# Kernel tuning notes

Measured on AMD Instinct MI355X. Metric: run time of the kernel, lower is better.

Reference implementation:

```python
import jax, jax.numpy as jnp
from jax import lax
import numpy as np

EPS_LN = 1e-5
EPS_BN = 1e-5
NEG_SLOPE = 0.01  # MONAI UnetResBlock leaky relu slope


def conv3d(x, w, b=None, padding=0, dilation=1, groups=1):
    # x: [B,C,D1,D2,D3], w: [O, I/groups, k,k,k]
    pads = [(padding, padding)] * 3
    y = lax.conv_general_dilated(x, w, (1, 1, 1), pads,
                                 rhs_dilation=(dilation,) * 3,
                                 dimension_numbers=('NCDHW', 'OIDHW', 'NCDHW'),
                                 feature_group_count=groups)
    if b is not None:
        y = y + b[None, :, None, None, None]
    return y


def _trilinear(x_flat, z, y, xw, D, H, W):
    # x_flat: [B,C,S]; z,y,xw: [B,S] float sample coords. Zero padding outside.
    z0 = jnp.floor(z); y0 = jnp.floor(y); x0 = jnp.floor(xw)
    tz = z - z0; ty = y - y0; tx = xw - x0
    iz0 = z0.astype(jnp.int32); iy0 = y0.astype(jnp.int32); ix0 = x0.astype(jnp.int32)
    gather = jax.vmap(lambda xf, i: jnp.take(xf, i, axis=1))  # over batch
    out = jnp.zeros_like(x_flat)
    for dz in (0, 1):
        for dy in (0, 1):
            for dx in (0, 1):
                zi = iz0 + dz; yi = iy0 + dy; xi = ix0 + dx
                wgt = ((tz if dz else 1.0 - tz) * (ty if dy else 1.0 - ty)
                       * (tx if dx else 1.0 - tx))
                valid = ((zi >= 0) & (zi < D) & (yi >= 0) & (yi < H)
                         & (xi >= 0) & (xi < W))
                idx = (jnp.clip(zi, 0, D - 1) * H + jnp.clip(yi, 0, H - 1)) * W \
                      + jnp.clip(xi, 0, W - 1)
                g = gather(x_flat, idx)  # [B,C,S]
                out = out + g * (wgt * valid)[:, None, :]
    return out


def deform_conv3d(x, off_w, off_b, w, b):
    # DCNv1-style 3D deformable conv, kernel 3x3x3, stride 1, pad 1.
    B, C, D, H, W = x.shape
    S = D * H * W
    off = conv3d(x, off_w, off_b, padding=1)          # [B, 3*27, D,H,W]
    off = off.reshape(B, 27, 3, S)                    # per-tap (dz,dy,dx)
    gz, gy, gx = jnp.meshgrid(jnp.arange(D), jnp.arange(H), jnp.arange(W), indexing='ij')
    gz = gz.reshape(-1).astype(x.dtype)
    gy = gy.reshape(-1).astype(x.dtype)
    gx = gx.reshape(-1).astype(x.dtype)
    x_flat = x.reshape(B, C, S)
    out = jnp.zeros((B, w.shape[0], S), x.dtype)
    k = 0
    for kd in (-1, 0, 1):
        for kh in (-1, 0, 1):
            for kw in (-1, 0, 1):
                z = gz[None, :] + kd + off[:, k, 0]
                y = gy[None, :] + kh + off[:, k, 1]
                xc = gx[None, :] + kw + off[:, k, 2]
                val = _trilinear(x_flat, z, y, xc, D, H, W)  # [B,C,S]
                out = out + jnp.einsum('oc,bcs->bos', w[:, :, kd + 1, kh + 1, kw + 1], val)
                k += 1
    out = out + b[None, :, None]
    return out.reshape(B, w.shape[0], D, H, W)


def _leaky(v):
    return jnp.where(v >= 0, v, NEG_SLOPE * v)


def _bn(v, s, b_, m, var):
    inv = lax.rsqrt(var + EPS_BN)
    return (v - m[None, :, None, None, None]) * (s * inv)[None, :, None, None, None] \
        + b_[None, :, None, None, None]


def reference(x, ln_s, ln_b, gamma,
              p1_w, p1_b, p2_w, p2_b,
              c0_w, c0_b, cs_w, cs_b,
              off_w, off_b, dc_w, dc_b,
              c1_w, c1_b,
              u1_w, bn1_s, bn1_b, bn1_m, bn1_v,
              u2_w, bn2_s, bn2_b, bn2_m, bn2_v,
              pr_w, pr_b):
    B, C, H, W, D = x.shape
    tok = x.reshape(B, C, -1).transpose(0, 2, 1)  # [B, N, C]
    # LayerNorm over C
    mu = jnp.mean(tok, axis=-1, keepdims=True)
    var = jnp.mean((tok - mu) ** 2, axis=-1, keepdims=True)
    xn = (tok - mu) * lax.rsqrt(var + EPS_LN) * ln_s + ln_b
    # _Attention3d_deform
    v = xn.transpose(0, 2, 1).reshape(B, C, H, W, D)
    shortcut = v
    v = conv3d(v, p1_w, p1_b)                 # proj_1 (1x1x1)
    v = jax.nn.gelu(v, approximate=False)
    # _3d_deform spatial gating unit
    u = v
    a = conv3d(v, c0_w, c0_b, padding=2, groups=C)              # 5x5x5 depthwise
    a = conv3d(a, cs_w, cs_b, padding=9, dilation=3, groups=C)  # 7x7x7 dil=3 depthwise
    a = deform_conv3d(a, off_w, off_b, dc_w, dc_b)
    a = conv3d(a, c1_w, c1_b)                 # 1x1x1
    v = u * a
    v = conv3d(v, p2_w, p2_b) + shortcut      # proj_2 + residual
    epa = v.reshape(B, C, -1).transpose(0, 2, 1)
    feat = tok + gamma * epa                  # [B, N, C]
    skip = feat.reshape(B, H, W, D, C).transpose(0, 4, 1, 2, 3)  # [B,C,H,W,D]
    # UnetResBlock (conv-bn-lrelu-conv-bn + residual, lrelu), eval-mode BN
    h = conv3d(skip, u1_w, padding=1)
    h = _leaky(_bn(h, bn1_s, bn1_b, bn1_m, bn1_v))
    h = conv3d(h, u2_w, padding=1)
    h = _bn(h, bn2_s, bn2_b, bn2_m, bn2_v)
    attn = _leaky(h + skip)
    # projconv: Dropout3d is identity in eval; 1x1x1 conv
    out = skip + conv3d(attn, pr_w, pr_b)
    return out


def setup_inputs() -> dict:
    key = jax.random.key(0)
    ks = jax.random.split(key, 16)
    C, Bv, S = 48, 2, 32

    def w(k, shape, s=0.05):
        return jax.random.normal(k, shape, jnp.float32) * s

    return {
        'x': jax.random.normal(ks[0], (Bv, C, S, S, S), jnp.float32),
        'ln_s': jnp.ones((C,), jnp.float32), 'ln_b': jnp.zeros((C,), jnp.float32),
        'gamma': jnp.full((C,), 0.1, jnp.float32),
        'p1_w': w(ks[1], (C, C, 1, 1, 1)), 'p1_b': jnp.zeros((C,), jnp.float32),
        'p2_w': w(ks[2], (C, C, 1, 1, 1)), 'p2_b': jnp.zeros((C,), jnp.float32),
        'c0_w': w(ks[3], (C, 1, 5, 5, 5)), 'c0_b': jnp.zeros((C,), jnp.float32),
        'cs_w': w(ks[4], (C, 1, 7, 7, 7)), 'cs_b': jnp.zeros((C,), jnp.float32),
        'off_w': w(ks[5], (81, C, 3, 3, 3), 0.01), 'off_b': jnp.zeros((81,), jnp.float32),
        'dc_w': w(ks[6], (C, C, 3, 3, 3)), 'dc_b': jnp.zeros((C,), jnp.float32),
        'c1_w': w(ks[7], (C, C, 1, 1, 1)), 'c1_b': jnp.zeros((C,), jnp.float32),
        'u1_w': w(ks[8], (C, C, 3, 3, 3)),
        'bn1_s': jnp.ones((C,), jnp.float32), 'bn1_b': jnp.zeros((C,), jnp.float32),
        'bn1_m': jnp.zeros((C,), jnp.float32), 'bn1_v': jnp.ones((C,), jnp.float32),
        'u2_w': w(ks[9], (C, C, 3, 3, 3)),
        'bn2_s': jnp.ones((C,), jnp.float32), 'bn2_b': jnp.zeros((C,), jnp.float32),
        'bn2_m': jnp.zeros((C,), jnp.float32), 'bn2_v': jnp.ones((C,), jnp.float32),
        'pr_w': w(ks[10], (C, C, 1, 1, 1)), 'pr_b': jnp.zeros((C,), jnp.float32),
    }
```

## Files before the change

kernel.cpp:

```cpp
#include <hip/hip_runtime.h>
#include <hip/hip_fp16.h>
#include <math.h>

#define CCH 48
#define SDIM 32
#define SVOL (SDIM*SDIM*SDIM)
#define NB 2

typedef _Float16 half2_t __attribute__((ext_vector_type(2)));
typedef _Float16 half4_t __attribute__((ext_vector_type(4)));
typedef float float4_t __attribute__((ext_vector_type(4)));

static __device__ __forceinline__ float dot2f(half2_t a, half2_t b, float c) {
#if __has_builtin(__builtin_amdgcn_fdot2)
    return __builtin_amdgcn_fdot2(a, b, c, false);
#else
    return c + (float)a[0] * (float)b[0] + (float)a[1] * (float)b[1];
#endif
}


__global__ __launch_bounds__(256)
void reshape_mfma_off_kernel(const float* __restrict__ w, half4_t* __restrict__ wA) {
    int e = blockIdx.x * 256 + threadIdx.x;
    if (e < 31104) {
        int row = e & 15;
        int kq = (e >> 4) & 3;
        int ks = (e / 64) % 3;
        int mt = (e / 192) % 6;
        int tap = e / 1152;
        int o = mt * 16 + row;
        half4_t v;
        #pragma unroll
        for (int h = 0; h < 4; h++) {
            int ci = ks * 16 + kq * 4 + h;
            float val = (o < 81) ? w[((size_t)o * CCH + ci) * 27 + tap] : 0.f;
            v[h] = (_Float16)val;
        }
        wA[e] = v;
    }
}

__global__ __launch_bounds__(256)
void reshape_mfma48_kernel(const float* __restrict__ w, half4_t* __restrict__ wA) {
    int e = blockIdx.x * 256 + threadIdx.x;
    if (e < 15552) {
        int row = e & 15;
        int kq = (e >> 4) & 3;
        int ks = (e / 64) % 3;
        int mt = (e / 192) % 3;
        int tap = e / 576;
        int o = mt * 16 + row;
        half4_t v;
        #pragma unroll
        for (int h = 0; h < 4; h++) {
            int ci = ks * 16 + kq * 4 + h;
            v[h] = (_Float16)w[((size_t)o * CCH + ci) * 27 + tap];
        }
        wA[e] = v;
    }
}

__global__ __launch_bounds__(256)
void reshape_mfma_dc_kernel(const float* __restrict__ w, half4_t* __restrict__ wA) {
    int e = blockIdx.x * 256 + threadIdx.x;
    if (e < 15552) {
        int row = e & 15;
        int kq = (e >> 4) & 3;
        int mt = (e / 64) % 3;
        int tap = (e / 192) % 27;
        int gc = e / 5184;
        int o = mt * 16 + row;
        half4_t v;
        #pragma unroll
        for (int h = 0; h < 4; h++) {
            int ci = gc * 16 + kq * 4 + h;
            v[h] = (_Float16)w[((size_t)o * CCH + ci) * 27 + tap];
        }
        wA[e] = v;
    }
}

__global__ __launch_bounds__(256)
void t1x1_pair_kernel(const float* __restrict__ w, half2_t* __restrict__ wt) {
    int i = blockIdx.x * 256 + threadIdx.x;
    if (i < 24 * CCH) {
        int o = i % CCH, cp = i / CCH;
        wt[i] = half2_t{ (_Float16)w[o * CCH + 2 * cp], (_Float16)w[o * CCH + 2 * cp + 1] };
    }
}

__global__ __launch_bounds__(256)
void t1x1_kernel(const float* __restrict__ w, float* __restrict__ wt) {
    int i = blockIdx.x * 256 + threadIdx.x;
    if (i < CCH * CCH) { int ci = i / CCH, o = i % CCH; wt[i] = w[o * CCH + ci]; }
}

__global__ __launch_bounds__(64)
void cb_kernel(const float* __restrict__ c1w, const float* __restrict__ c1b,
               const float* __restrict__ dcb, float* __restrict__ cb) {
    int o = threadIdx.x;
    if (o < CCH) {
        float v = c1b[o];
        for (int ci = 0; ci < CCH; ci++) v += c1w[o * CCH + ci] * dcb[ci];
        cb[o] = v;
    }
}

__global__ __launch_bounds__(256)
void ln_kernel(const float* __restrict__ x, const float* __restrict__ ln_s,
               const float* __restrict__ ln_b, float* __restrict__ xn,
               half2_t* __restrict__ xnp) {
    int s = blockIdx.x * 256 + threadIdx.x;
    int b = blockIdx.y;
    const float* xb = x + (size_t)b * CCH * SVOL + s;
    float v[CCH];
    float mu = 0.f;
    #pragma unroll
    for (int c = 0; c < CCH; c++) { v[c] = xb[c * SVOL]; mu += v[c]; }
    mu *= (1.0f / CCH);
    float var = 0.f;
    #pragma unroll
    for (int c = 0; c < CCH; c++) { float d = v[c] - mu; var += d * d; }
    var *= (1.0f / CCH);
    float inv = rsqrtf(var + 1e-5f);
    float* o = xn + (size_t)b * CCH * SVOL + s;
    float nv[CCH];
    #pragma unroll
    for (int c = 0; c < CCH; c++) { nv[c] = (v[c] - mu) * inv * ln_s[c] + ln_b[c]; o[c * SVOL] = nv[c]; }
    half2_t* xp = xnp + (size_t)b * 24 * SVOL + s;
    #pragma unroll
    for (int cp = 0; cp < 24; cp++)
        xp[(size_t)cp * SVOL] = half2_t{ (_Float16)nv[2 * cp], (_Float16)nv[2 * cp + 1] };
}

__global__ __launch_bounds__(256, 4)
void p1_gelu_kernel(const half2_t* __restrict__ xnp, const half2_t* __restrict__ wt,
                    const float* __restrict__ bias, float* __restrict__ u) {
    int tid = threadIdx.x;
    int g = blockIdx.y, b = blockIdx.z;
    int s = blockIdx.x * 256 + tid;
    const half2_t* xb = xnp + (size_t)b * 24 * SVOL + s;
    float acc[12];
    #pragma unroll
    for (int o = 0; o < 12; o++) acc[o] = bias[g * 12 + o];
    for (int cp = 0; cp < 24; cp++) {
        half2_t v2 = xb[(size_t)cp * SVOL];
        const half2_t* wr = wt + cp * CCH + g * 12;
        #pragma unroll
        for (int o = 0; o < 12; o++) acc[o] = dot2f(v2, wr[o], acc[o]);
    }
    float* ub = u + (size_t)b * CCH * SVOL + s + (size_t)(g * 12) * SVOL;
    #pragma unroll
    for (int o = 0; o < 12; o++) {
        float a = acc[o];
        ub[o * SVOL] = 0.5f * a * (1.0f + erff(a * 0.70710678118654752f));
    }
}

__global__ __launch_bounds__(256, 4)
void dw5_kernel(const float* __restrict__ in, const float* __restrict__ w,
                const float* __restrict__ bias, float* __restrict__ out) {
    int tid = threadIdx.x;
    int c = blockIdx.y, b = blockIdx.z;
    const float* wc = w + c * 125;
    int bx = blockIdx.x;
    int yx = (bx >> 1) * 256 + tid;
    int z0 = (bx & 1) * 16;
    int y = yx >> 5, xx = yx & 31;
    const float* ib = in + ((size_t)b * CCH + c) * SVOL;
    float acc[16];
    float bv = bias[c];
    #pragma unroll
    for (int z = 0; z < 16; z++) acc[z] = bv;
    for (int ty = 0; ty < 5; ty++) {
        int yy = y + ty - 2; if (yy < 0 || yy >= 32) continue;
        for (int tx = 0; tx < 5; tx++) {
            int xv = xx + tx - 2; if (xv < 0 || xv >= 32) continue;
            const float* col = ib + yy * 32 + xv;
            float cv[20];
            #pragma unroll
            for (int j = 0; j < 20; j++) {
                int zz = z0 - 2 + j;
                cv[j] = (zz >= 0 && zz < 32) ? col[(size_t)zz * 1024] : 0.f;
            }
            #pragma unroll
            for (int tz = 0; tz < 5; tz++) {
                float wv = wc[(tz * 5 + ty) * 5 + tx];
                #pragma unroll
                for (int z = 0; z < 16; z++) acc[z] += wv * cv[z + tz];
            }
        }
    }
    float* ob = out + ((size_t)b * CCH + c) * SVOL + y * 32 + xx;
    #pragma unroll
    for (int z = 0; z < 16; z++) ob[(size_t)(z0 + z) * 1024] = acc[z];
}

__global__ __launch_bounds__(256, 4)
void dw7_kernel(const float* __restrict__ in, const float* __restrict__ w,
                const float* __restrict__ bias, float* __restrict__ out) {
    int tid = threadIdx.x;
    int c = blockIdx.y, b = blockIdx.z;
    const float* wc = w + c * 343;
    int bx = blockIdx.x;
    int yx = (bx >> 1) * 256 + tid;
    int z0 = (bx & 1) * 16;
    int y = yx >> 5, xx = yx & 31;
    const float* ib = in + ((size_t)b * CCH + c) * SVOL;
    float acc[16];
    float bv = bias[c];
    #pragma unroll
    for (int z = 0; z < 16; z++) acc[z] = bv;
    for (int ty = 0; ty < 7; ty++) {
        int yy = y + 3 * (ty - 3); if (yy < 0 || yy >= 32) continue;
        for (int tx = 0; tx < 7; tx++) {
            int xv = xx + 3 * (tx - 3); if (xv < 0 || xv >= 32) continue;
            const float* col = ib + yy * 32 + xv;
            float cv[34];
            #pragma unroll
            for (int j = 0; j < 34; j++) {
                int zz = z0 - 9 + j;
                cv[j] = (zz >= 0 && zz < 32) ? col[(size_t)zz * 1024] : 0.f;
            }
            #pragma unroll
            for (int tz = 0; tz < 7; tz++) {
                float wv = wc[(tz * 7 + ty) * 7 + tx];
                #pragma unroll
                for (int z = 0; z < 16; z++) acc[z] += wv * cv[z + 3 * tz];
            }
        }
    }
    float* ob = out + ((size_t)b * CCH + c) * SVOL + y * 32 + xx;
    #pragma unroll
    for (int z = 0; z < 16; z++) ob[(size_t)(z0 + z) * 1024] = acc[z];
}

__global__ __launch_bounds__(256)
void transpose_pack_kernel(const float* __restrict__ a1, __half* __restrict__ a1h) {
    __shared__ float tile[CCH * 65];
    int tid = threadIdx.x;
    int b = blockIdx.y;
    int s0 = blockIdx.x * 64;
    const float* ib = a1 + (size_t)b * CCH * SVOL + s0;
    for (int i = tid; i < CCH * 64; i += 256) {
        int c = i >> 6, p = i & 63;
        tile[c * 65 + p] = ib[(size_t)c * SVOL + p];
    }
    __syncthreads();
    __half* ob = a1h + ((size_t)b * SVOL + s0) * CCH;
    for (int i = tid; i < 64 * CCH; i += 256) {
        int p = i / CCH, c = i % CCH;
        ob[i] = __float2half(tile[c * 65 + p]);
    }
}

__global__ __launch_bounds__(256, 4)
void offconv_mfma_kernel(const __half* __restrict__ a1h, const half4_t* __restrict__ wA,
                         float* __restrict__ off) {
    __shared__ __half halo[216 * 52];
    int tid = threadIdx.x;
    int t = blockIdx.x;
    int b = blockIdx.y;
    int tz0 = (t >> 6) * 4, ty0 = ((t >> 3) & 7) * 4, tx0 = (t & 7) * 4;
    const __half* ab = a1h + (size_t)b * SVOL * CCH;
    for (int idx = tid; idx < 216 * 24; idx += 256) {
        int hpos = idx / 24, kp = idx % 24;
        int hz = hpos / 36, hy = (hpos / 6) % 6, hx = hpos % 6;
        int gz = tz0 + hz - 1, gy = ty0 + hy - 1, gx = tx0 + hx - 1;
        unsigned int v = 0u;
        if (gz >= 0 && gz < 32 && gy >= 0 && gy < 32 && gx >= 0 && gx < 32) {
            int s = (gz * 32 + gy) * 32 + gx;
            v = *reinterpret_cast<const unsigned int*>(ab + (size_t)s * CCH + kp * 2);
        }
        *reinterpret_cast<unsigned int*>(&halo[hpos * 52 + kp * 2]) = v;
    }
    __syncthreads();
    int wave = tid >> 6, lane = tid & 63;
    int col = lane & 15;
    int kq = lane >> 4;
    int py = col >> 2, px = col & 3;
    int pz = wave;
    float4_t acc[6];
    #pragma unroll
    for (int m = 0; m < 6; m++) acc[m] = (float4_t)0.f;
    for (int tap = 0; tap < 27; tap++) {
        int dz = tap / 9, dy = (tap / 3) % 3, dx = tap % 3;
        int hbase = ((pz + dz) * 36 + (py + dy) * 6 + (px + dx)) * 52 + kq * 4;
        half4_t bf0 = *reinterpret_cast<const half4_t*>(&halo[hbase]);
        half4_t bf1 = *reinterpret_cast<const half4_t*>(&halo[hbase + 16]);
        half4_t bf2 = *reinterpret_cast<const half4_t*>(&halo[hbase + 32]);
        #pragma unroll
        for (int mt = 0; mt < 6; mt++) {
            int fb = (tap * 6 + mt) * 12 + kq;
            half4_t a0 = wA[(size_t)fb * 16 + col];
            half4_t a1 = wA[(size_t)(fb + 4) * 16 + col];
            half4_t a2 = wA[(size_t)(fb + 8) * 16 + col];
            acc[mt] = __builtin_amdgcn_mfma_f32_16x16x16f16(a0, bf0, acc[mt], 0, 0, 0);
            acc[mt] = __builtin_amdgcn_mfma_f32_16x16x16f16(a1, bf1, acc[mt], 0, 0, 0);
            acc[mt] = __builtin_amdgcn_mfma_f32_16x16x16f16(a2, bf2, acc[mt], 0, 0, 0);
        }
    }
    int sg = ((tz0 + pz) * 32 + ty0 + py) * 32 + tx0 + px;
    float* ob = off + (size_t)b * 81 * SVOL + sg;
    #pragma unroll
    for (int mt = 0; mt < 6; mt++) {
        #pragma unroll
        for (int r = 0; r < 4; r++) {
            int orow = mt * 16 + kq * 4 + r;
            if (orow < 81) ob[(size_t)orow * SVOL] = acc[mt][r];
        }
    }
}

__global__ __launch_bounds__(256, 4)
void u1_mfma_kernel(const __half* __restrict__ skh, const half4_t* __restrict__ wA,
                    const float* __restrict__ bs, const float* __restrict__ bb,
                    const float* __restrict__ bm, const float* __restrict__ bv,
                    __half* __restrict__ h1h) {
    __shared__ __half halo[216 * 52];
    int tid = threadIdx.x;
    int t = blockIdx.x;
    int b = blockIdx.y;
    int tz0 = (t >> 6) * 4, ty0 = ((t >> 3) & 7) * 4, tx0 = (t & 7) * 4;
    const __half* ab = skh + (size_t)b * SVOL * CCH;
    for (int idx = tid; idx < 216 * 24; idx += 256) {
        int hpos = idx / 24, kp = idx % 24;
        int hz = hpos / 36, hy = (hpos / 6) % 6, hx = hpos % 6;
        int gz = tz0 + hz - 1, gy = ty0 + hy - 1, gx = tx0 + hx - 1;
        unsigned int v = 0u;
        if (gz >= 0 && gz < 32 && gy >= 0 && gy < 32 && gx >= 0 && gx < 32) {
            int s = (gz * 32 + gy) * 32 + gx;
            v = *reinterpret_cast<const unsigned int*>(ab + (size_t)s * CCH + kp * 2);
        }
        *reinterpret_cast<unsigned int*>(&halo[hpos * 52 + kp * 2]) = v;
    }
    __syncthreads();
    int wave = tid >> 6, lane = tid & 63;
    int col = lane & 15;
    int kq = lane >> 4;
    int py = col >> 2, px = col & 3;
    int pz = wave;
    float4_t acc[3];
    #pragma unroll
    for (int m = 0; m < 3; m++) acc[m] = (float4_t)0.f;
    for (int tap = 0; tap < 27; tap++) {
        int dz = tap / 9, dy = (tap / 3) % 3, dx = tap % 3;
        int hbase = ((pz + dz) * 36 + (py + dy) * 6 + (px + dx)) * 52 + kq * 4;
        half4_t bf0 = *reinterpret_cast<const half4_t*>(&halo[hbase]);
        half4_t bf1 = *reinterpret_cast<const half4_t*>(&halo[hbase + 16]);
        half4_t bf2 = *reinterpret_cast<const half4_t*>(&halo[hbase + 32]);
        #pragma unroll
        for (int mt = 0; mt < 3; mt++) {
            int fb = (tap * 3 + mt) * 12 + kq;
            half4_t a0 = wA[(size_t)fb * 16 + col];
            half4_t a1 = wA[(size_t)(fb + 4) * 16 + col];
            half4_t a2 = wA[(size_t)(fb + 8) * 16 + col];
            acc[mt] = __builtin_amdgcn_mfma_f32_16x16x16f16(a0, bf0, acc[mt], 0, 0, 0);
            acc[mt] = __builtin_amdgcn_mfma_f32_16x16x16f16(a1, bf1, acc[mt], 0, 0, 0);
            acc[mt] = __builtin_amdgcn_mfma_f32_16x16x16f16(a2, bf2, acc[mt], 0, 0, 0);
        }
    }
    int sg = ((tz0 + pz) * 32 + ty0 + py) * 32 + tx0 + px;
    __half* ob = h1h + ((size_t)b * SVOL + sg) * CCH;
    #pragma unroll
    for (int mt = 0; mt < 3; mt++) {
        float hv[4];
        #pragma unroll
        for (int r = 0; r < 4; r++) {
            int orow = mt * 16 + kq * 4 + r;
            float inv = rsqrtf(bv[orow] + 1e-5f);
            float h = (acc[mt][r] - bm[orow]) * (bs[orow] * inv) + bb[orow];
            hv[r] = h >= 0.f ? h : 0.01f * h;
        }
        half2_t* po = reinterpret_cast<half2_t*>(ob + mt * 16 + kq * 4);
        po[0] = half2_t{ (_Float16)hv[0], (_Float16)hv[1] };
        po[1] = half2_t{ (_Float16)hv[2], (_Float16)hv[3] };
    }
}

__global__ __launch_bounds__(256, 4)
void u2_mfma_kernel(const __half* __restrict__ h1h, const float* __restrict__ skip,
                    const half4_t* __restrict__ wA,
                    const float* __restrict__ bs, const float* __restrict__ bb,
                    const float* __restrict__ bm, const float* __restrict__ bv,
                    __half* __restrict__ attnh) {
    __shared__ __half halo[216 * 52];
    int tid = threadIdx.x;
    int t = blockIdx.x;
    int b = blockIdx.y;
    int tz0 = (t >> 6) * 4, ty0 = ((t >> 3) & 7) * 4, tx0 = (t & 7) * 4;
    const __half* ab = h1h + (size_t)b * SVOL * CCH;
    for (int idx = tid; idx < 216 * 24; idx += 256) {
        int hpos = idx / 24, kp = idx % 24;
        int hz = hpos / 36, hy = (hpos / 6) % 6, hx = hpos % 6;
        int gz = tz0 + hz - 1, gy = ty0 + hy - 1, gx = tx0 + hx - 1;
        unsigned int v = 0u;
        if (gz >= 0 && gz < 32 && gy >= 0 && gy < 32 && gx >= 0 && gx < 32) {
            int s = (gz * 32 + gy) * 32 + gx;
            v = *reinterpret_cast<const unsigned int*>(ab + (size_t)s * CCH + kp * 2);
        }
        *reinterpret_cast<unsigned int*>(&halo[hpos * 52 + kp * 2]) = v;
    }
    __syncthreads();
    int wave = tid >> 6, lane = tid & 63;
    int col = lane & 15;
    int kq = lane >> 4;
    int py = col >> 2, px = col & 3;
    int pz = wave;
    float4_t acc[3];
    #pragma unroll
    for (int m = 0; m < 3; m++) acc[m] = (float4_t)0.f;
    for (int tap = 0; tap < 27; tap++) {
        int dz = tap / 9, dy = (tap / 3) % 3, dx = tap % 3;
        int hbase = ((pz + dz) * 36 + (py + dy) * 6 + (px + dx)) * 52 + kq * 4;
        half4_t bf0 = *reinterpret_cast<const half4_t*>(&halo[hbase]);
        half4_t bf1 = *reinterpret_cast<const half4_t*>(&halo[hbase + 16]);
        half4_t bf2 = *reinterpret_cast<const half4_t*>(&halo[hbase + 32]);
        #pragma unroll
        for (int mt = 0; mt < 3; mt++) {
            int fb = (tap * 3 + mt) * 12 + kq;
            half4_t a0 = wA[(size_t)fb * 16 + col];
            half4_t a1 = wA[(size_t)(fb + 4) * 16 + col];
            half4_t a2 = wA[(size_t)(fb + 8) * 16 + col];
            acc[mt] = __builtin_amdgcn_mfma_f32_16x16x16f16(a0, bf0, acc[mt], 0, 0, 0);
            acc[mt] = __builtin_amdgcn_mfma_f32_16x16x16f16(a1, bf1, acc[mt], 0, 0, 0);
            acc[mt] = __builtin_amdgcn_mfma_f32_16x16x16f16(a2, bf2, acc[mt], 0, 0, 0);
        }
    }
    int sg = ((tz0 + pz) * 32 + ty0 + py) * 32 + tx0 + px;
    const float* sk = skip + (size_t)b * CCH * SVOL + sg;
    __half* ob = attnh + ((size_t)b * SVOL + sg) * CCH;
    #pragma unroll
    for (int mt = 0; mt < 3; mt++) {
        float av[4];
        #pragma unroll
        for (int r = 0; r < 4; r++) {
            int orow = mt * 16 + kq * 4 + r;
            float inv = rsqrtf(bv[orow] + 1e-5f);
            float h = (acc[mt][r] - bm[orow]) * (bs[orow] * inv) + bb[orow];
            float a = h + sk[(size_t)orow * SVOL];
            av[r] = a >= 0.f ? a : 0.01f * a;
        }
        half2_t* po = reinterpret_cast<half2_t*>(ob + mt * 16 + kq * 4);
        po[0] = half2_t{ (_Float16)av[0], (_Float16)av[1] };
        po[1] = half2_t{ (_Float16)av[2], (_Float16)av[3] };
    }
}

struct h8v { half2_t a, b, c, d; };

__global__ __launch_bounds__(64)
void deform_mfma_kernel(const __half* __restrict__ a1h, const float* __restrict__ off,
                        const float* __restrict__ off_b,
                        const half4_t* __restrict__ wA, float* __restrict__ out) {
    __shared__ __half vbuf[2][64][20];
    int lane = threadIdx.x;
    int gc = blockIdx.y;
    int b = blockIdx.z;
    int col = lane & 15, kq = lane >> 4;
    int s = blockIdx.x * 64 + lane;
    int z = s >> 10, y = (s >> 5) & 31, xx = s & 31;
    const __half* abase = a1h + (size_t)b * SVOL * CCH + gc * 16;
    const float* ob = off + (size_t)b * 81 * SVOL + s;
    float4_t acc[3][4];
    #pragma unroll
    for (int m = 0; m < 3; m++)
        #pragma unroll
        for (int c = 0; c < 4; c++) acc[m][c] = (float4_t)0.f;
    for (int k = 0; k < 27; k++) {
        int kd = k / 9 - 1, kh = (k / 3) % 3 - 1, kw = k % 3 - 1;
        float zf = (float)(z + kd) + ob[(size_t)(k * 3 + 0) * SVOL] + off_b[k * 3 + 0];
        float yf = (float)(y + kh) + ob[(size_t)(k * 3 + 1) * SVOL] + off_b[k * 3 + 1];
        float xf = (float)(xx + kw) + ob[(size_t)(k * 3 + 2) * SVOL] + off_b[k * 3 + 2];
        float z0 = floorf(zf), y0 = floorf(yf), x0 = floorf(xf);
        float tz = zf - z0, ty = yf - y0, tx = xf - x0;
        int iz0 = (int)z0, iy0 = (int)y0, ix0 = (int)x0;
        half2_t val2[8];
        #pragma unroll
        for (int j = 0; j < 8; j++) val2[j] = (half2_t)(_Float16)0;
        #pragma unroll
        for (int corner = 0; corner < 8; corner++) {
            int dz = corner >> 2, dy = (corner >> 1) & 1, dx = corner & 1;
            int zi = iz0 + dz, yi = iy0 + dy, xi = ix0 + dx;
            bool valid = (zi >= 0 && zi < 32 && yi >= 0 && yi < 32 && xi >= 0 && xi < 32);
            float wgt = (dz ? tz : 1.f - tz) * (dy ? ty : 1.f - ty) * (dx ? tx : 1.f - tx);
            float cwv = valid ? wgt : 0.f;
            _Float16 cwh = (_Float16)cwv;
            half2_t cw2 = { cwh, cwh };
            int zc = min(max(zi, 0), 31), yc = min(max(yi, 0), 31), xc = min(max(xi, 0), 31);
            int cidx = (zc * 32 + yc) * 32 + xc;
            const h8v* pv = (const h8v*)(abase + (size_t)cidx * CCH);
            h8v q0 = pv[0], q1 = pv[1];
            val2[0] += cw2 * q0.a;  val2[1] += cw2 * q0.b;
            val2[2] += cw2 * q0.c;  val2[3] += cw2 * q0.d;
            val2[4] += cw2 * q1.a;  val2[5] += cw2 * q1.b;
            val2[6] += cw2 * q1.c;  val2[7] += cw2 * q1.d;
        }
        __half* vb = &vbuf[k & 1][lane][0];
        half4_t* vb4 = reinterpret_cast<half4_t*>(vb);
        vb4[0] = half4_t{ val2[0][0], val2[0][1], val2[1][0], val2[1][1] };
        vb4[1] = half4_t{ val2[2][0], val2[2][1], val2[3][0], val2[3][1] };
        vb4[2] = half4_t{ val2[4][0], val2[4][1], val2[5][0], val2[5][1] };
        vb4[3] = half4_t{ val2[6][0], val2[6][1], val2[7][0], val2[7][1] };
        half4_t a0, a1, a2;
        {
            int fb = ((gc * 27 + k) * 3 + 0) * 4 + kq;
            a0 = wA[(size_t)fb * 16 + col];
            a1 = wA[(size_t)(fb + 4) * 16 + col];
            a2 = wA[(size_t)(fb + 8) * 16 + col];
        }
        #pragma unroll
        for (int ct = 0; ct < 4; ct++) {
            half4_t bf = *reinterpret_cast<const half4_t*>(&vbuf[k & 1][ct * 16 + col][kq * 4]);
            acc[0][ct] = __builtin_amdgcn_mfma_f32_16x16x16f16(a0, bf, acc[0][ct], 0, 0, 0);
            acc[1][ct] = __builtin_amdgcn_mfma_f32_16x16x16f16(a1, bf, acc[1][ct], 0, 0, 0);
            acc[2][ct] = __builtin_amdgcn_mfma_f32_16x16x16f16(a2, bf, acc[2][ct], 0, 0, 0);
        }
    }
    int sbase = blockIdx.x * 64;
    float* op = out + (size_t)b * CCH * SVOL;
    #pragma unroll
    for (int mt = 0; mt < 3; mt++) {
        #pragma unroll
        for (int ct = 0; ct < 4; ct++) {
            int sp = sbase + ct * 16 + col;
            #pragma unroll
            for (int r = 0; r < 4; r++) {
                int o = mt * 16 + kq * 4 + r;
                atomicAdd(&op[(size_t)o * SVOL + sp], acc[mt][ct][r]);
            }
        }
    }
}

__global__ __launch_bounds__(256, 4)
void gate1_kernel(const float* __restrict__ dc, const float* __restrict__ u,
                  const float* __restrict__ wt, const float* __restrict__ cb,
                  half2_t* __restrict__ a2p) {
    int tid = threadIdx.x;
    int g = blockIdx.y, b = blockIdx.z;
    int s = blockIdx.x * 256 + tid;
    size_t base = (size_t)b * CCH * SVOL + s;
    float acc[12];
    #pragma unroll
    for (int o = 0; o < 12; o++) acc[o] = cb[g * 12 + o];
    for (int ci = 0; ci < CCH; ci++) {
        float v = dc[base + (size_t)ci * SVOL];
        const float* wr = wt + ci * CCH + g * 12;
        #pragma unroll
        for (int o = 0; o < 12; o++) acc[o] += wr[o] * v;
    }
    #pragma unroll
    for (int o = 0; o < 12; o++) acc[o] *= u[base + (size_t)(g * 12 + o) * SVOL];
    half2_t* ap = a2p + ((size_t)b * 24 + g * 6) * SVOL + s;
    #pragma unroll
    for (int j = 0; j < 6; j++)
        ap[(size_t)j * SVOL] = half2_t{ (_Float16)acc[2 * j], (_Float16)acc[2 * j + 1] };
}

__global__ __launch_bounds__(256, 4)
void gate2_kernel(const half2_t* __restrict__ a2p, const float* __restrict__ xn,
                  const float* __restrict__ x,
                  const half2_t* __restrict__ wt, const float* __restrict__ p2b,
                  const float* __restrict__ gamma, float* __restrict__ skip,
                  __half* __restrict__ skh) {
    int tid = threadIdx.x;
    int g = blockIdx.y, b = blockIdx.z;
    int s = blockIdx.x * 256 + tid;
    size_t base = (size_t)b * CCH * SVOL + s;
    const half2_t* ab = a2p + (size_t)b * 24 * SVOL + s;
    float acc[12];
    #pragma unroll
    for (int o = 0; o < 12; o++) acc[o] = p2b[g * 12 + o];
    for (int cp = 0; cp < 24; cp++) {
        half2_t v2 = ab[(size_t)cp * SVOL];
        const half2_t* wr = wt + cp * CCH + g * 12;
        #pragma unroll
        for (int o = 0; o < 12; o++) acc[o] = dot2f(v2, wr[o], acc[o]);
    }
    float sv[12];
    #pragma unroll
    for (int o = 0; o < 12; o++) {
        int oc = g * 12 + o;
        float vv = acc[o] + xn[base + (size_t)oc * SVOL];
        sv[o] = x[base + (size_t)oc * SVOL] + gamma[oc] * vv;
        skip[base + (size_t)oc * SVOL] = sv[o];
    }
    half2_t* sh = reinterpret_cast<half2_t*>(skh + ((size_t)b * SVOL + s) * CCH + g * 12);
    #pragma unroll
    for (int j = 0; j < 6; j++)
        sh[j] = half2_t{ (_Float16)sv[2 * j], (_Float16)sv[2 * j + 1] };
}

__global__ __launch_bounds__(256, 4)
void pr_final_kernel(const __half* __restrict__ attnh, const float* __restrict__ skip,
                     const half2_t* __restrict__ wt, const float* __restrict__ prb,
                     float* __restrict__ out) {
    int tid = threadIdx.x;
    int g = blockIdx.y, b = blockIdx.z;
    int s = blockIdx.x * 256 + tid;
    size_t base = (size_t)b * CCH * SVOL + s;
    const half2_t* ab = reinterpret_cast<const half2_t*>(attnh + ((size_t)b * SVOL + s) * CCH);
    float acc[12];
    #pragma unroll
    for (int o = 0; o < 12; o++) acc[o] = prb[g * 12 + o];
    for (int cp = 0; cp < 24; cp++) {
        half2_t v2 = ab[cp];
        const half2_t* wr = wt + cp * CCH + g * 12;
        #pragma unroll
        for (int o = 0; o < 12; o++) acc[o] = dot2f(v2, wr[o], acc[o]);
    }
    #pragma unroll
    for (int o = 0; o < 12; o++) {
        int oc = g * 12 + o;
        out[base + (size_t)oc * SVOL] = skip[base + (size_t)oc * SVOL] + acc[o];
    }
}

extern "C" void kernel_launch(void* const* d_in, const int* in_sizes, int n_in,
                              void* d_out, int out_size, void* d_ws, size_t ws_size,
                              hipStream_t stream) {
    (void)in_sizes; (void)n_in; (void)out_size; (void)ws_size;
    const float* x     = (const float*)d_in[0];
    const float* ln_s  = (const float*)d_in[1];
    const float* ln_b  = (const float*)d_in[2];
    const float* gamma = (const float*)d_in[3];
    const float* p1_w  = (const float*)d_in[4];
    const float* p1_b  = (const float*)d_in[5];
    const float* p2_w  = (const float*)d_in[6];
    const float* p2_b  = (const float*)d_in[7];
    const float* c0_w  = (const float*)d_in[8];
    const float* c0_b  = (const float*)d_in[9];
    const float* cs_w  = (const float*)d_in[10];
    const float* cs_b  = (const float*)d_in[11];
    const float* off_w = (const float*)d_in[12];
    const float* off_b = (const float*)d_in[13];
    const float* dc_w  = (const float*)d_in[14];
    const float* dc_b  = (const float*)d_in[15];
    const float* c1_w  = (const float*)d_in[16];
    const float* c1_b  = (const float*)d_in[17];
    const float* u1_w  = (const float*)d_in[18];
    const float* bn1_s = (const float*)d_in[19];
    const float* bn1_b = (const float*)d_in[20];
    const float* bn1_m = (const float*)d_in[21];
    const float* bn1_v = (const float*)d_in[22];
    const float* u2_w  = (const float*)d_in[23];
    const float* bn2_s = (const float*)d_in[24];
    const float* bn2_b = (const float*)d_in[25];
    const float* bn2_m = (const float*)d_in[26];
    const float* bn2_v = (const float*)d_in[27];
    const float* pr_w  = (const float*)d_in[28];
    const float* pr_b  = (const float*)d_in[29];
    float* out = (float*)d_out;

    float* wsf = (float*)d_ws;
    const size_t TS = (size_t)NB * CCH * SVOL;
    float* xn   = out;
    float* ubuf = wsf;
    float* bufA = wsf + TS;
    float* bufB = wsf + 2 * TS;
    float* offb = wsf + 3 * TS;
    float* wtb    = wsf + 3 * TS + (size_t)NB * 81 * SVOL;
    float* wt_offf = wtb;
    float* wt_dcf  = wt_offf + 104976;
    float* wt_u1f  = wt_dcf + 62208;
    float* wt_u2f  = wt_u1f + 62208;
    float* pt_p1  = wt_u2f + 62208;
    float* pt_c1  = pt_p1 + 2304;
    float* pt_p2  = pt_c1 + 2304;
    float* pt_pr  = pt_p2 + 2304;
    float* cb_all = pt_pr + 2304;

    __half*  a1h = (__half*)bufA;
    __half*  skh = (__half*)ubuf;
    __half*  h1h = (__half*)(ubuf + TS / 2);
    half2_t* xnp = (half2_t*)bufB;
    half2_t* a2p = (half2_t*)offb;
    __half*  attnh = (__half*)offb;
    half4_t* wA_off = (half4_t*)wt_offf;
    half4_t* wA_dc  = (half4_t*)wt_dcf;
    half4_t* wA_u1 = (half4_t*)wt_u1f;
    half4_t* wA_u2 = (half4_t*)wt_u2f;
    half2_t* wt_p1h  = (half2_t*)pt_p1;
    half2_t* wt_p2h  = (half2_t*)pt_p2;
    half2_t* wt_prh  = (half2_t*)pt_pr;

    dim3 blk(256);
    dim3 gpos(SVOL / 256, NB);
    dim3 g4(SVOL / 256, 4, NB);
    dim3 gmf(512, NB);
    dim3 g1w(SVOL / 64, 3, NB);
    dim3 gdwc(8, CCH, NB);
    dim3 gtr(SVOL / 64, NB);

    hipLaunchKernelGGL(reshape_mfma_off_kernel, dim3((31104 + 255) / 256), blk, 0, stream, off_w, wA_off);
    hipLaunchKernelGGL(reshape_mfma48_kernel, dim3((15552 + 255) / 256), blk, 0, stream, u1_w, wA_u1);
    hipLaunchKernelGGL(reshape_mfma48_kernel, dim3((15552 + 255) / 256), blk, 0, stream, u2_w, wA_u2);
    hipLaunchKernelGGL(reshape_mfma_dc_kernel, dim3((15552 + 255) / 256), blk, 0, stream, dc_w, wA_dc);
    hipLaunchKernelGGL(t1x1_pair_kernel, dim3(5), blk, 0, stream, p1_w, wt_p1h);
    hipLaunchKernelGGL(t1x1_pair_kernel, dim3(5), blk, 0, stream, p2_w, wt_p2h);
    hipLaunchKernelGGL(t1x1_pair_kernel, dim3(5), blk, 0, stream, pr_w, wt_prh);
    hipLaunchKernelGGL(t1x1_kernel, dim3(9), blk, 0, stream, c1_w, pt_c1);
    hipLaunchKernelGGL(cb_kernel, dim3(1), dim3(64), 0, stream, c1_w, c1_b, dc_b, cb_all);

    hipLaunchKernelGGL(ln_kernel,            gpos, blk, 0, stream, x, ln_s, ln_b, xn, xnp);
    hipLaunchKernelGGL(p1_gelu_kernel,       g4,   blk, 0, stream, xnp, wt_p1h, p1_b, ubuf);
    hipLaunchKernelGGL(dw5_kernel,           gdwc, blk, 0, stream, ubuf, c0_w, c0_b, bufA);
    hipLaunchKernelGGL(dw7_kernel,           gdwc, blk, 0, stream, bufA, cs_w, cs_b, bufB);
    hipLaunchKernelGGL(transpose_pack_kernel, gtr, blk, 0, stream, bufB, a1h);
    hipLaunchKernelGGL(offconv_mfma_kernel,  gmf,  blk, 0, stream, a1h, wA_off, offb);
    hipMemsetAsync(bufB, 0, TS * sizeof(float), stream);
    hipLaunchKernelGGL(deform_mfma_kernel,   g1w,  dim3(64), 0, stream, a1h, offb, off_b, wA_dc, bufB);
    hipLaunchKernelGGL(gate1_kernel,         g4,   blk, 0, stream, bufB, ubuf, pt_c1, cb_all, a2p);
    hipLaunchKernelGGL(gate2_kernel,         g4,   blk, 0, stream, a2p, xn, x, wt_p2h, p2_b, gamma,
                       bufA, skh);
    hipLaunchKernelGGL(u1_mfma_kernel,       gmf,  blk, 0, stream, skh, wA_u1,
                       bn1_s, bn1_b, bn1_m, bn1_v, h1h);
    hipLaunchKernelGGL(u2_mfma_kernel,       gmf,  blk, 0, stream, h1h, bufA, wA_u2,
                       bn2_s, bn2_b, bn2_m, bn2_v, attnh);
    hipLaunchKernelGGL(pr_final_kernel,      g4,   blk, 0, stream, attnh, bufA, wt_prh, pr_b, out);
}
```

Measured before the change: 483.4 us.

## Stage 8x8x8 halo tile in LDS for deformable conv bilinear gathers

```diff
diff --git a/kernel.cpp b/kernel.cpp
--- a/kernel.cpp
+++ b/kernel.cpp
@@ -448,20 +448,34 @@
     }
 }
 
-struct h8v { half2_t a, b, c, d; };
-
 __global__ __launch_bounds__(64)
 void deform_mfma_kernel(const __half* __restrict__ a1h, const float* __restrict__ off,
                         const float* __restrict__ off_b,
                         const half4_t* __restrict__ wA, float* __restrict__ out) {
+    __shared__ __half halo[512 * 20];
     __shared__ __half vbuf[2][64][20];
     int lane = threadIdx.x;
+    int t = blockIdx.x;
     int gc = blockIdx.y;
     int b = blockIdx.z;
+    int tz0 = (t >> 6) * 4, ty0 = ((t >> 3) & 7) * 4, tx0 = (t & 7) * 4;
     int col = lane & 15, kq = lane >> 4;
-    int s = blockIdx.x * 64 + lane;
-    int z = s >> 10, y = (s >> 5) & 31, xx = s & 31;
     const __half* abase = a1h + (size_t)b * SVOL * CCH + gc * 16;
+    for (int i = lane; i < 512; i += 64) {
+        int hz = i >> 6, hy = (i >> 3) & 7, hx = i & 7;
+        int gz = tz0 - 2 + hz, gy = ty0 - 2 + hy, gx = tx0 - 2 + hx;
+        half4_t v0 = (half4_t)(_Float16)0, v1 = v0, v2 = v0, v3 = v0;
+        if (gz >= 0 && gz < 32 && gy >= 0 && gy < 32 && gx >= 0 && gx < 32) {
+            const half4_t* p = reinterpret_cast<const half4_t*>(
+                abase + (size_t)((gz * 32 + gy) * 32 + gx) * CCH);
+            v0 = p[0]; v1 = p[1]; v2 = p[2]; v3 = p[3];
+        }
+        half4_t* d = reinterpret_cast<half4_t*>(&halo[i * 20]);
+        d[0] = v0; d[1] = v1; d[2] = v2; d[3] = v3;
+    }
+    int pz = lane >> 4, py = (lane >> 2) & 3, px = lane & 3;
+    int s = ((tz0 + pz) * 32 + (ty0 + py)) * 32 + (tx0 + px);
+    int z = tz0 + pz, y = ty0 + py, xx = tx0 + px;
     const float* ob = off + (size_t)b * 81 * SVOL + s;
     float4_t acc[3][4];
     #pragma unroll
@@ -476,9 +490,9 @@
         float z0 = floorf(zf), y0 = floorf(yf), x0 = floorf(xf);
         float tz = zf - z0, ty = yf - y0, tx = xf - x0;
         int iz0 = (int)z0, iy0 = (int)y0, ix0 = (int)x0;
-        half2_t val2[8];
-        #pragma unroll
-        for (int j = 0; j < 8; j++) val2[j] = (half2_t)(_Float16)0;
+        half4_t val4[4];
+        #pragma unroll
+        for (int j = 0; j < 4; j++) val4[j] = (half4_t)(_Float16)0;
         #pragma unroll
         for (int corner = 0; corner < 8; corner++) {
             int dz = corner >> 2, dy = (corner >> 1) & 1, dx = corner & 1;
@@ -487,22 +501,24 @@
             float wgt = (dz ? tz : 1.f - tz) * (dy ? ty : 1.f - ty) * (dx ? tx : 1.f - tx);
             float cwv = valid ? wgt : 0.f;
             _Float16 cwh = (_Float16)cwv;
-            half2_t cw2 = { cwh, cwh };
+            half4_t cw4 = { cwh, cwh, cwh, cwh };
             int zc = min(max(zi, 0), 31), yc = min(max(yi, 0), 31), xc = min(max(xi, 0), 31);
-            int cidx = (zc * 32 + yc) * 32 + xc;
-            const h8v* pv = (const h8v*)(abase + (size_t)cidx * CCH);
-            h8v q0 = pv[0], q1 = pv[1];
-            val2[0] += cw2 * q0.a;  val2[1] += cw2 * q0.b;
-            val2[2] += cw2 * q0.c;  val2[3] += cw2 * q0.d;
-            val2[4] += cw2 * q1.a;  val2[5] += cw2 * q1.b;
-            val2[6] += cw2 * q1.c;  val2[7] += cw2 * q1.d;
-        }
-        __half* vb = &vbuf[k & 1][lane][0];
-        half4_t* vb4 = reinterpret_cast<half4_t*>(vb);
-        vb4[0] = half4_t{ val2[0][0], val2[0][1], val2[1][0], val2[1][1] };
-        vb4[1] = half4_t{ val2[2][0], val2[2][1], val2[3][0], val2[3][1] };
-        vb4[2] = half4_t{ val2[4][0], val2[4][1], val2[5][0], val2[5][1] };
-        vb4[3] = half4_t{ val2[6][0], val2[6][1], val2[7][0], val2[7][1] };
+            int hz = zc - tz0 + 2, hy = yc - ty0 + 2, hx = xc - tx0 + 2;
+            half4_t q0, q1, q2, q3;
+            if ((unsigned)hz < 8u && (unsigned)hy < 8u && (unsigned)hx < 8u) {
+                const half4_t* pl = reinterpret_cast<const half4_t*>(
+                    &halo[((hz * 8 + hy) * 8 + hx) * 20]);
+                q0 = pl[0]; q1 = pl[1]; q2 = pl[2]; q3 = pl[3];
+            } else {
+                const half4_t* pg = reinterpret_cast<const half4_t*>(
+                    abase + (size_t)((zc * 32 + yc) * 32 + xc) * CCH);
+                q0 = pg[0]; q1 = pg[1]; q2 = pg[2]; q3 = pg[3];
+            }
+            val4[0] += cw4 * q0;  val4[1] += cw4 * q1;
+            val4[2] += cw4 * q2;  val4[3] += cw4 * q3;
+        }
+        half4_t* vb4 = reinterpret_cast<half4_t*>(&vbuf[k & 1][lane][0]);
+        vb4[0] = val4[0]; vb4[1] = val4[1]; vb4[2] = val4[2]; vb4[3] = val4[3];
         half4_t a0, a1, a2;
         {
             int fb = ((gc * 27 + k) * 3 + 0) * 4 + kq;
@@ -518,13 +534,14 @@
             acc[2][ct] = __builtin_amdgcn_mfma_f32_16x16x16f16(a2, bf, acc[2][ct], 0, 0, 0);
         }
     }
-    int sbase = blockIdx.x * 64;
     float* op = out + (size_t)b * CCH * SVOL;
     #pragma unroll
     for (int mt = 0; mt < 3; mt++) {
         #pragma unroll
         for (int ct = 0; ct < 4; ct++) {
-            int sp = sbase + ct * 16 + col;
+            int posidx = ct * 16 + col;
+            int qz = posidx >> 4, qy = (posidx >> 2) & 3, qx = posidx & 3;
+            int sp = ((tz0 + qz) * 32 + (ty0 + qy)) * 32 + (tx0 + qx);
             #pragma unroll
             for (int r = 0; r < 4; r++) {
                 int o = mt * 16 + kq * 4 + r;
@@ -690,7 +707,7 @@
     dim3 gpos(SVOL / 256, NB);
     dim3 g4(SVOL / 256, 4, NB);
     dim3 gmf(512, NB);
-    dim3 g1w(SVOL / 64, 3, NB);
+    dim3 gdf(512, 3, NB);
     dim3 gdwc(8, CCH, NB);
     dim3 gtr(SVOL / 64, NB);
 
@@ -711,7 +728,7 @@
     hipLaunchKernelGGL(transpose_pack_kernel, gtr, blk, 0, stream, bufB, a1h);
     hipLaunchKernelGGL(offconv_mfma_kernel,  gmf,  blk, 0, stream, a1h, wA_off, offb);
     hipMemsetAsync(bufB, 0, TS * sizeof(float), stream);
-    hipLaunchKernelGGL(deform_mfma_kernel,   g1w,  dim3(64), 0, stream, a1h, offb, off_b, wA_dc, bufB);
+    hipLaunchKernelGGL(deform_mfma_kernel,   gdf,  dim3(64), 0, stream, a1h, offb, off_b, wA_dc, bufB);
     hipLaunchKernelGGL(gate1_kernel,         g4,   blk, 0, stream, bufB, ubuf, pt_c1, cb_all, a2p);
     hipLaunchKernelGGL(gate2_kernel,         g4,   blk, 0, stream, a2p, xn, x, wt_p2h, p2_b, gamma,
                        bufA, skh);
```

Measured after the change: 604.3 us. +25.0%, slower.
